# Kernel tuning notes

Hardware: AMD Instinct MI355X
Metric: run time of the kernel (lower is better)

Reference implementation:

```python
import jax, jax.numpy as jnp
import numpy as np

B, S, D = 8, 1024, 256
H, DH = 8, 32  # num_heads, head_dim; H*DH == D


def setup_inputs() -> dict:
    key = jax.random.key(0)
    ks = jax.random.split(key, 10)
    s = 0.02
    return {
        "q": jax.random.normal(ks[0], (B, S, D), jnp.float32),
        "k": jax.random.normal(ks[1], (B, S, D), jnp.float32),
        "v": jax.random.normal(ks[2], (B, S, D), jnp.float32),
        "mask": jnp.zeros((B, 1, 1, S), jnp.float32),  # additive mask
        "bias": jax.random.normal(ks[3], (1, H, S, S), jnp.float32),  # pair bias
        "Wq": jax.random.normal(ks[4], (H * DH, D), jnp.float32) * s,
        "Wk": jax.random.normal(ks[5], (H * DH, D), jnp.float32) * s,
        "Wv": jax.random.normal(ks[6], (H * DH, D), jnp.float32) * s,
        "Wg": jnp.zeros((H * DH, D), jnp.float32),   # gating init: zeros weight
        "bg": jnp.ones((H * DH,), jnp.float32),      # gating init: ones bias
        "Wo": jax.random.normal(ks[7], (D, H * DH), jnp.float32) * s,
    }


def reference(q, k, v, mask, bias, Wq, Wk, Wv, Wg, bg, Wo):
    norm = DH ** -0.5
    g = jnp.einsum('bsd,ed->bse', q, Wg) + bg            # [B,S,H*DH]
    qh = (jnp.einsum('bsd,ed->bse', q, Wq) * norm).reshape(B, S, H, DH)
    kh = jnp.einsum('bsd,ed->bse', k, Wk).reshape(B, S, H, DH)
    vh = jnp.einsum('bsd,ed->bse', v, Wv).reshape(B, S, H, DH)
    # scores [B,H,Q,K] with additive mask and pair bias (unicore softmax_dropout)
    attn = jnp.einsum('bqhd,bkhd->bhqk', qh, kh) + mask + bias
    attn = jax.nn.softmax(attn, axis=-1)
    o = jnp.einsum('bhqk,bkhd->bqhd', attn, vh).reshape(B, S, H * DH)
    o = jax.nn.sigmoid(g) * o                            # gating
    return jnp.einsum('bse,de->bsd', o, Wo)              # output proj, NO bias in fwd
```

## Files before the change

### kernel.cpp

```cpp
#include <hip/hip_runtime.h>


typedef __attribute__((ext_vector_type(4))) float f32x4;
typedef __attribute__((ext_vector_type(8))) unsigned short u16x8;
typedef __attribute__((ext_vector_type(4))) unsigned short u16x4;
typedef __attribute__((ext_vector_type(8))) __bf16 bf16x8;
typedef __attribute__((ext_vector_type(4))) __bf16 bf16x4;

#define BB 8
#define SS 1024
#define DD 256
#define HH 8
#define DHD 32

__device__ __forceinline__ float b2f(unsigned short s) {
  unsigned u = ((unsigned)s) << 16;
  return __builtin_bit_cast(float, u);
}
__device__ __forceinline__ f32x4 mfma16(u16x8 a, u16x8 b, f32x4 c) {
  return __builtin_amdgcn_mfma_f32_16x16x32_bf16(
      __builtin_bit_cast(bf16x8, a), __builtin_bit_cast(bf16x8, b), c, 0, 0, 0);
}

__global__ __launch_bounds__(256) void proj_kernel(
    const float* __restrict__ q, const float* __restrict__ k,
    const float* __restrict__ v,
    const float* __restrict__ Wq, const float* __restrict__ Wg,
    const float* __restrict__ Wk, const float* __restrict__ Wv,
    const float* __restrict__ bg,
    unsigned short* __restrict__ qh, unsigned short* __restrict__ kh,
    unsigned short* __restrict__ vhT, unsigned short* __restrict__ sig) {
  const int slot = blockIdx.z;
  const float* A = (slot <= 1) ? q : (slot == 2 ? k : v);
  const float* W = (slot == 0) ? Wq : (slot == 1 ? Wg : (slot == 2 ? Wk : Wv));
  const int row0 = blockIdx.x * 64, col0 = blockIdx.y * 64;
  const int tid = threadIdx.x;
  const int w = tid >> 6, lane = tid & 63, g = lane >> 4, c = lane & 15;
  const int sr = tid >> 2, sc = tid & 3;

  __shared__ alignas(16) unsigned short As[64 * 32];
  __shared__ alignas(16) unsigned short Ws[64 * 32];

  const f32x4 zero = {0.f, 0.f, 0.f, 0.f};
  f32x4 acc[4] = {zero, zero, zero, zero};

  for (int kk = 0; kk < 8; ++kk) {
    __syncthreads();
    {
      const float* ap = A + (size_t)(row0 + sr) * DD + kk * 32 + sc * 8;
      f32x4 f0 = *(const f32x4*)ap;
      f32x4 f1 = *(const f32x4*)(ap + 4);
      bf16x8 a8;
#pragma unroll
      for (int j = 0; j < 4; ++j) { a8[j] = (__bf16)f0[j]; a8[j + 4] = (__bf16)f1[j]; }
      ((u16x8*)As)[sr * 4 + (sc ^ ((sr >> 1) & 3))] = __builtin_bit_cast(u16x8, a8);

      const float* wp = W + (size_t)(col0 + sr) * DD + kk * 32 + sc * 8;
      f32x4 w0 = *(const f32x4*)wp;
      f32x4 w1 = *(const f32x4*)(wp + 4);
      bf16x8 w8;
#pragma unroll
      for (int j = 0; j < 4; ++j) { w8[j] = (__bf16)w0[j]; w8[j + 4] = (__bf16)w1[j]; }
      ((u16x8*)Ws)[sr * 4 + (sc ^ ((sr >> 1) & 3))] = __builtin_bit_cast(u16x8, w8);
    }
    __syncthreads();
    const int arow = 16 * w + c;
    u16x8 af = ((u16x8*)As)[arow * 4 + (g ^ ((arow >> 1) & 3))];
#pragma unroll
    for (int n = 0; n < 4; ++n) {
      const int brow = 16 * n + c;
      u16x8 wf = ((u16x8*)Ws)[brow * 4 + (g ^ ((brow >> 1) & 3))];
      acc[n] = mfma16(af, wf, acc[n]);
    }
  }

  if (slot == 3) {
    const int row_base = row0 + 16 * w + 4 * g;
    const int bb = row_base >> 10;
    const int s0 = row_base & 1023;
#pragma unroll
    for (int n = 0; n < 4; ++n) {
      const int col = col0 + 16 * n + c;
      bf16x4 pv;
#pragma unroll
      for (int r = 0; r < 4; ++r) pv[r] = (__bf16)acc[n][r];
      *(u16x4*)(vhT + (size_t)(bb * 256 + col) * SS + s0) =
          __builtin_bit_cast(u16x4, pv);
    }
  } else {
#pragma unroll
    for (int n = 0; n < 4; ++n) {
#pragma unroll
      for (int r = 0; r < 4; ++r) {
        const int row = row0 + 16 * w + 4 * g + r;
        const int col = col0 + 16 * n + c;
        const size_t idx = (size_t)row * DD + col;
        const float val = acc[n][r];
        if (slot == 0)
          qh[idx] = __builtin_bit_cast(unsigned short,
                        (__bf16)(val * 0.17677669529663687f));
        else if (slot == 1)
          sig[idx] = __builtin_bit_cast(unsigned short,
                         (__bf16)(1.0f / (1.0f + __expf(-(val + bg[col])))));
        else
          kh[idx] = __builtin_bit_cast(unsigned short, (__bf16)val);
      }
    }
  }
}

__global__ __launch_bounds__(256) void attn_kernel(
    const unsigned short* __restrict__ qh, const unsigned short* __restrict__ kh,
    const unsigned short* __restrict__ vhT, const unsigned short* __restrict__ sig,
    const float* __restrict__ mask, const float* __restrict__ bias,
    unsigned short* __restrict__ og) {
  const int bid = blockIdx.x;
  const int widx = (bid & 7) * 128 + (bid >> 3);
  const int h = widx >> 7, b = (widx >> 4) & 7, qt = widx & 15;
  const int tid = threadIdx.x;
  const int w = tid >> 6, lane = tid & 63, g = lane >> 4, c = lane & 15;

  __shared__ alignas(16) unsigned short Ks[64 * 32];
  __shared__ alignas(16) unsigned short Vt[32 * 64];
  __shared__ alignas(16) unsigned short Ps[4][16 * 64];
  u16x8* Ks16 = (u16x8*)Ks;
  u16x8* Vt16 = (u16x8*)Vt;
  unsigned short* P = Ps[w];

  const int q0 = qt * 64 + w * 16;
  const u16x8 qf =
      *(const u16x8*)(qh + (size_t)(b * SS + q0 + c) * DD + h * DHD + g * 8);

  const f32x4 zero = {0.f, 0.f, 0.f, 0.f};
  f32x4 acc[2] = {zero, zero};
  float m_r = -1e30f, l_r = 0.f;

  const float* maskb = mask + b * SS;
  const float* biasb = bias + (size_t)(h * SS + q0 + c) * SS;

  const int krow = tid >> 2, kj = tid & 3;
  const int vrow = tid >> 3, vj = tid & 7;
  const unsigned short* kg =
      kh + (size_t)(b * SS + krow) * DD + h * DHD + kj * 8;
  const unsigned short* vg =
      vhT + (size_t)((b * HH + h) * DHD + vrow) * SS + vj * 8;
  const int kslot = krow * 4 + (kj ^ ((krow >> 1) & 3));
  const int vslot = vrow * 8 + (vj ^ (vrow & 7));

  Ks16[kslot] = *(const u16x8*)kg;
  Vt16[vslot] = *(const u16x8*)vg;
  __syncthreads();

  for (int kt = 0; kt < 16; ++kt) {
    const int kv0 = kt * 64;
    u16x8 kreg, vreg;
    if (kt < 15) {
      kreg = *(const u16x8*)(kg + (size_t)(kv0 + 64) * DD);
      vreg = *(const u16x8*)(vg + kv0 + 64);
    }

    f32x4 sv[4];
#pragma unroll
    for (int t = 0; t < 4; ++t) {
      const u16x8 kf = Ks16[(16 * t + c) * 4 + (g ^ ((c >> 1) & 3))];
      sv[t] = mfma16(kf, qf, zero);
    }
#pragma unroll
    for (int t = 0; t < 4; ++t) {
      const f32x4 bi = *(const f32x4*)(biasb + kv0 + 16 * t + 4 * g);
      const f32x4 mk = *(const f32x4*)(maskb + kv0 + 16 * t + 4 * g);
#pragma unroll
      for (int r = 0; r < 4; ++r) sv[t][r] += mk[r] + bi[r];
    }
    float mx = fmaxf(fmaxf(sv[0][0], sv[0][1]), fmaxf(sv[0][2], sv[0][3]));
#pragma unroll
    for (int t = 1; t < 4; ++t)
      mx = fmaxf(mx, fmaxf(fmaxf(sv[t][0], sv[t][1]), fmaxf(sv[t][2], sv[t][3])));
    mx = fmaxf(mx, __shfl_xor(mx, 16));
    mx = fmaxf(mx, __shfl_xor(mx, 32));
    const float mnew = fmaxf(m_r, mx);
    const float scale = __expf(m_r - mnew);
    float ps = 0.f;
#pragma unroll
    for (int t = 0; t < 4; ++t)
#pragma unroll
      for (int r = 0; r < 4; ++r) {
        const float p = __expf(sv[t][r] - mnew);
        sv[t][r] = p;
        ps += p;
      }
    ps += __shfl_xor(ps, 16);
    ps += __shfl_xor(ps, 32);
    l_r = l_r * scale + ps;
    m_r = mnew;
    acc[0] *= scale;
    acc[1] *= scale;
#pragma unroll
    for (int t = 0; t < 4; ++t) {
      bf16x4 pv;
#pragma unroll
      for (int r = 0; r < 4; ++r) pv[r] = (__bf16)sv[t][r];
      const int n = 2 * t + (g >> 1);
      *(u16x4*)(P + c * 64 + ((n ^ (c & 7)) << 3) + ((g & 1) << 2)) =
          __builtin_bit_cast(u16x4, pv);
    }
#pragma unroll
    for (int s2 = 0; s2 < 2; ++s2) {
      const u16x8 pf =
          *(const u16x8*)(P + c * 64 + (((4 * s2 + g) ^ (c & 7)) << 3));
#pragma unroll
      for (int dt = 0; dt < 2; ++dt) {
        const u16x8 vf =
            Vt16[(16 * dt + c) * 8 + ((s2 * 4 + g) ^ (c & 7))];
        acc[dt] = mfma16(vf, pf, acc[dt]);
      }
    }
    if (kt < 15) {
      __syncthreads();
      Ks16[kslot] = kreg;
      Vt16[vslot] = vreg;
      __syncthreads();
    }
  }

  const float inv = 1.0f / l_r;
#pragma unroll
  for (int dt = 0; dt < 2; ++dt) {
    const size_t idx =
        (size_t)(b * SS + q0 + c) * DD + h * DHD + 16 * dt + 4 * g;
    const u16x4 sg = *(const u16x4*)(sig + idx);
    bf16x4 ov;
#pragma unroll
    for (int r = 0; r < 4; ++r) ov[r] = (__bf16)(acc[dt][r] * inv * b2f(sg[r]));
    *(u16x4*)(og + idx) = __builtin_bit_cast(u16x4, ov);
  }
}

__global__ __launch_bounds__(256) void outproj_kernel(
    const unsigned short* __restrict__ og, const float* __restrict__ Wo,
    float* __restrict__ out) {
  const int row0 = blockIdx.x * 64, col0 = blockIdx.y * 64;
  const int tid = threadIdx.x;
  const int w = tid >> 6, lane = tid & 63, g = lane >> 4, c = lane & 15;
  const int sr = tid >> 2, sc = tid & 3;

  __shared__ alignas(16) unsigned short As[64 * 32];
  __shared__ alignas(16) unsigned short Ws[64 * 32];

  const f32x4 zero = {0.f, 0.f, 0.f, 0.f};
  f32x4 acc[4] = {zero, zero, zero, zero};

  for (int kk = 0; kk < 8; ++kk) {
    __syncthreads();
    {
      const unsigned short* ap = og + (size_t)(row0 + sr) * DD + kk * 32 + sc * 8;
      ((u16x8*)As)[sr * 4 + (sc ^ ((sr >> 1) & 3))] = *(const u16x8*)ap;

      const float* wp = Wo + (size_t)(col0 + sr) * DD + kk * 32 + sc * 8;
      f32x4 w0 = *(const f32x4*)wp;
      f32x4 w1 = *(const f32x4*)(wp + 4);
      bf16x8 w8;
#pragma unroll
      for (int j = 0; j < 4; ++j) { w8[j] = (__bf16)w0[j]; w8[j + 4] = (__bf16)w1[j]; }
      ((u16x8*)Ws)[sr * 4 + (sc ^ ((sr >> 1) & 3))] = __builtin_bit_cast(u16x8, w8);
    }
    __syncthreads();
    const int arow = 16 * w + c;
    u16x8 af = ((u16x8*)As)[arow * 4 + (g ^ ((arow >> 1) & 3))];
#pragma unroll
    for (int n = 0; n < 4; ++n) {
      const int brow = 16 * n + c;
      u16x8 wf = ((u16x8*)Ws)[brow * 4 + (g ^ ((brow >> 1) & 3))];
      acc[n] = mfma16(af, wf, acc[n]);
    }
  }

#pragma unroll
  for (int n = 0; n < 4; ++n) {
#pragma unroll
    for (int r = 0; r < 4; ++r) {
      const int row = row0 + 16 * w + 4 * g + r;
      const int col = col0 + 16 * n + c;
      out[(size_t)row * DD + col] = acc[n][r];
    }
  }
}

extern "C" void kernel_launch(void* const* d_in, const int* in_sizes, int n_in,
                              void* d_out, int out_size, void* d_ws,
                              size_t ws_size, hipStream_t stream) {
  const float* q    = (const float*)d_in[0];
  const float* k    = (const float*)d_in[1];
  const float* v    = (const float*)d_in[2];
  const float* mask = (const float*)d_in[3];
  const float* bias = (const float*)d_in[4];
  const float* Wq   = (const float*)d_in[5];
  const float* Wk   = (const float*)d_in[6];
  const float* Wv   = (const float*)d_in[7];
  const float* Wg   = (const float*)d_in[8];
  const float* bg   = (const float*)d_in[9];
  const float* Wo   = (const float*)d_in[10];
  float* out = (float*)d_out;

  char* ws = (char*)d_ws;
  unsigned short* qh  = (unsigned short*)(ws);
  unsigned short* kh  = (unsigned short*)(ws + (4u << 20));
  unsigned short* vhT = (unsigned short*)(ws + (8u << 20));
  unsigned short* sig = (unsigned short*)(ws + (12u << 20));
  unsigned short* og  = (unsigned short*)(ws + (16u << 20));

  hipLaunchKernelGGL(proj_kernel, dim3(128, 4, 4), dim3(256), 0, stream,
                     q, k, v, Wq, Wg, Wk, Wv, bg, qh, kh, vhT, sig);
  hipLaunchKernelGGL(attn_kernel, dim3(1024), dim3(256), 0, stream,
                     qh, kh, vhT, sig, mask, bias, og);
  hipLaunchKernelGGL(outproj_kernel, dim3(128, 4), dim3(256), 0, stream,
                     og, Wo, out);
}
```

Measured before the change: 77.29 us.

## Split attention KV range across two wave groups and merge partial softmax

```diff
diff --git a/kernel.cpp b/kernel.cpp
--- a/kernel.cpp
+++ b/kernel.cpp
@@ -109,7 +109,7 @@
   }
 }
 
-__global__ __launch_bounds__(256) void attn_kernel(
+__global__ __launch_bounds__(512, 8) void attn_kernel(
     const unsigned short* __restrict__ qh, const unsigned short* __restrict__ kh,
     const unsigned short* __restrict__ vhT, const unsigned short* __restrict__ sig,
     const float* __restrict__ mask, const float* __restrict__ bias,
@@ -119,15 +119,17 @@
   const int h = widx >> 7, b = (widx >> 4) & 7, qt = widx & 15;
   const int tid = threadIdx.x;
   const int w = tid >> 6, lane = tid & 63, g = lane >> 4, c = lane & 15;
-
-  __shared__ alignas(16) unsigned short Ks[64 * 32];
-  __shared__ alignas(16) unsigned short Vt[32 * 64];
-  __shared__ alignas(16) unsigned short Ps[4][16 * 64];
-  u16x8* Ks16 = (u16x8*)Ks;
-  u16x8* Vt16 = (u16x8*)Vt;
+  const int grp = w >> 2, wq = w & 3;
+
+  __shared__ alignas(16) unsigned short Ks[2][64 * 32];
+  __shared__ alignas(16) unsigned short Vt[2][32 * 64];
+  __shared__ alignas(16) unsigned short Ps[8][16 * 64];
+  __shared__ float MLs[4][16][2];
+  u16x8* Ks16 = (u16x8*)Ks[grp];
+  u16x8* Vt16 = (u16x8*)Vt[grp];
   unsigned short* P = Ps[w];
 
-  const int q0 = qt * 64 + w * 16;
+  const int q0 = qt * 64 + wq * 16;
   const u16x8 qf =
       *(const u16x8*)(qh + (size_t)(b * SS + q0 + c) * DD + h * DHD + g * 8);
 
@@ -135,15 +137,17 @@
   f32x4 acc[2] = {zero, zero};
   float m_r = -1e30f, l_r = 0.f;
 
-  const float* maskb = mask + b * SS;
-  const float* biasb = bias + (size_t)(h * SS + q0 + c) * SS;
-
-  const int krow = tid >> 2, kj = tid & 3;
-  const int vrow = tid >> 3, vj = tid & 7;
+  const int kvbase = grp * 512;
+  const float* maskb = mask + b * SS + kvbase;
+  const float* biasb = bias + (size_t)(h * SS + q0 + c) * SS + kvbase;
+
+  const int ltid = tid & 255;
+  const int krow = ltid >> 2, kj = ltid & 3;
+  const int vrow = ltid >> 3, vj = ltid & 7;
   const unsigned short* kg =
-      kh + (size_t)(b * SS + krow) * DD + h * DHD + kj * 8;
+      kh + (size_t)(b * SS + kvbase + krow) * DD + h * DHD + kj * 8;
   const unsigned short* vg =
-      vhT + (size_t)((b * HH + h) * DHD + vrow) * SS + vj * 8;
+      vhT + (size_t)((b * HH + h) * DHD + vrow) * SS + kvbase + vj * 8;
   const int kslot = krow * 4 + (kj ^ ((krow >> 1) & 3));
   const int vslot = vrow * 8 + (vj ^ (vrow & 7));
 
@@ -151,10 +155,11 @@
   Vt16[vslot] = *(const u16x8*)vg;
   __syncthreads();
 
-  for (int kt = 0; kt < 16; ++kt) {
+#pragma unroll 1
+  for (int kt = 0; kt < 8; ++kt) {
     const int kv0 = kt * 64;
     u16x8 kreg, vreg;
-    if (kt < 15) {
+    if (kt < 7) {
       kreg = *(const u16x8*)(kg + (size_t)(kv0 + 64) * DD);
       vreg = *(const u16x8*)(vg + kv0 + 64);
     }
@@ -169,32 +174,32 @@
     for (int t = 0; t < 4; ++t) {
       const f32x4 bi = *(const f32x4*)(biasb + kv0 + 16 * t + 4 * g);
       const f32x4 mk = *(const f32x4*)(maskb + kv0 + 16 * t + 4 * g);
-#pragma unroll
-      for (int r = 0; r < 4; ++r) sv[t][r] += mk[r] + bi[r];
-    }
-    float mx = fmaxf(fmaxf(sv[0][0], sv[0][1]), fmaxf(sv[0][2], sv[0][3]));
+      sv[t] += bi + mk;
+    }
+    float pm = fmaxf(fmaxf(sv[0][0], sv[0][1]), fmaxf(sv[0][2], sv[0][3]));
 #pragma unroll
     for (int t = 1; t < 4; ++t)
-      mx = fmaxf(mx, fmaxf(fmaxf(sv[t][0], sv[t][1]), fmaxf(sv[t][2], sv[t][3])));
-    mx = fmaxf(mx, __shfl_xor(mx, 16));
-    mx = fmaxf(mx, __shfl_xor(mx, 32));
-    const float mnew = fmaxf(m_r, mx);
-    const float scale = __expf(m_r - mnew);
+      pm = fmaxf(pm, fmaxf(fmaxf(sv[t][0], sv[t][1]), fmaxf(sv[t][2], sv[t][3])));
+    if (!__all(pm - m_r <= 8.0f)) {
+      float mx = fmaxf(pm, __shfl_xor(pm, 16));
+      mx = fmaxf(mx, __shfl_xor(mx, 32));
+      const float mnew = fmaxf(m_r, mx);
+      const float scale = __expf(m_r - mnew);
+      l_r *= scale;
+      acc[0] *= scale;
+      acc[1] *= scale;
+      m_r = mnew;
+    }
     float ps = 0.f;
 #pragma unroll
     for (int t = 0; t < 4; ++t)
 #pragma unroll
       for (int r = 0; r < 4; ++r) {
-        const float p = __expf(sv[t][r] - mnew);
+        const float p = __expf(sv[t][r] - m_r);
         sv[t][r] = p;
         ps += p;
       }
-    ps += __shfl_xor(ps, 16);
-    ps += __shfl_xor(ps, 32);
-    l_r = l_r * scale + ps;
-    m_r = mnew;
-    acc[0] *= scale;
-    acc[1] *= scale;
+    l_r += ps;
 #pragma unroll
     for (int t = 0; t < 4; ++t) {
       bf16x4 pv;
@@ -210,12 +215,11 @@
           *(const u16x8*)(P + c * 64 + (((4 * s2 + g) ^ (c & 7)) << 3));
 #pragma unroll
       for (int dt = 0; dt < 2; ++dt) {
-        const u16x8 vf =
-            Vt16[(16 * dt + c) * 8 + ((s2 * 4 + g) ^ (c & 7))];
+        const u16x8 vf = Vt16[(16 * dt + c) * 8 + ((s2 * 4 + g) ^ (c & 7))];
         acc[dt] = mfma16(vf, pf, acc[dt]);
       }
     }
-    if (kt < 15) {
+    if (kt < 7) {
       __syncthreads();
       Ks16[kslot] = kreg;
       Vt16[vslot] = vreg;
@@ -223,16 +227,38 @@
     }
   }
 
-  const float inv = 1.0f / l_r;
-#pragma unroll
-  for (int dt = 0; dt < 2; ++dt) {
-    const size_t idx =
-        (size_t)(b * SS + q0 + c) * DD + h * DHD + 16 * dt + 4 * g;
-    const u16x4 sg = *(const u16x4*)(sig + idx);
-    bf16x4 ov;
-#pragma unroll
-    for (int r = 0; r < 4; ++r) ov[r] = (__bf16)(acc[dt][r] * inv * b2f(sg[r]));
-    *(u16x4*)(og + idx) = __builtin_bit_cast(u16x4, ov);
+  float l_w = l_r + __shfl_xor(l_r, 16);
+  l_w += __shfl_xor(l_w, 32);
+
+  if (grp == 1) {
+    float* MB = (float*)Ps[w];
+#pragma unroll
+    for (int dt = 0; dt < 2; ++dt)
+#pragma unroll
+      for (int r = 0; r < 4; ++r)
+        MB[c * 32 + (((4 * dt + g) ^ (c & 7)) << 2) + r] = acc[dt][r];
+    if (g == 0) { MLs[wq][c][0] = m_r; MLs[wq][c][1] = l_w; }
+  }
+  __syncthreads();
+  if (grp == 0) {
+    const float m1 = MLs[wq][c][0], l1 = MLs[wq][c][1];
+    const float* MB = (const float*)Ps[w + 4];
+    const float M = fmaxf(m_r, m1);
+    const float e0 = __expf(m_r - M), e1 = __expf(m1 - M);
+    const float inv = 1.0f / (l_w * e0 + l1 * e1);
+#pragma unroll
+    for (int dt = 0; dt < 2; ++dt) {
+      const f32x4 a1 =
+          *(const f32x4*)(MB + c * 32 + (((4 * dt + g) ^ (c & 7)) << 2));
+      const size_t idx =
+          (size_t)(b * SS + q0 + c) * DD + h * DHD + 16 * dt + 4 * g;
+      const u16x4 sg = *(const u16x4*)(sig + idx);
+      bf16x4 ov;
+#pragma unroll
+      for (int r = 0; r < 4; ++r)
+        ov[r] = (__bf16)((acc[dt][r] * e0 + a1[r] * e1) * inv * b2f(sg[r]));
+      *(u16x4*)(og + idx) = __builtin_bit_cast(u16x4, ov);
+    }
   }
 }
 
@@ -311,7 +337,7 @@
 
   hipLaunchKernelGGL(proj_kernel, dim3(128, 4, 4), dim3(256), 0, stream,
                      q, k, v, Wq, Wg, Wk, Wv, bg, qh, kh, vhT, sig);
-  hipLaunchKernelGGL(attn_kernel, dim3(1024), dim3(256), 0, stream,
+  hipLaunchKernelGGL(attn_kernel, dim3(1024), dim3(512), 0, stream,
                      qh, kh, vhT, sig, mask, bias, og);
   hipLaunchKernelGGL(outproj_kernel, dim3(128, 4), dim3(256), 0, stream,
                      og, Wo, out);
```

Result: slower. 102.8 us (+32.9%).
